# Kernel tuning notes

Hardware: AMD Instinct MI355X
Metric: run time of the kernel (lower is better)

The kernel has to match this reference:

```python
import jax, jax.numpy as jnp
import numpy as np

STATE_DIM = 1024
INPUT_DIM = 1024
BATCH = 8192


def setup_inputs() -> dict:
    key = jax.random.key(0)
    ks = jax.random.split(key, 7)
    # Kaiming-uniform-ish init like torch Linear
    bx = 1.0 / np.sqrt(INPUT_DIM)
    bh = 1.0 / np.sqrt(STATE_DIM)
    return {
        "x": jax.random.normal(ks[0], (BATCH, INPUT_DIM), jnp.float32),
        "prevh": jax.random.normal(ks[1], (BATCH, STATE_DIM), jnp.float32),
        "prevc": jax.random.normal(ks[2], (BATCH, STATE_DIM), jnp.float32),
        "Wx": jax.random.uniform(ks[3], (INPUT_DIM, 4 * STATE_DIM), jnp.float32, -bx, bx),
        "bx": jax.random.uniform(ks[4], (4 * STATE_DIM,), jnp.float32, -bx, bx),
        "Wh": jax.random.uniform(ks[5], (STATE_DIM, 4 * STATE_DIM), jnp.float32, -bh, bh),
    }


def reference(x, prevh, prevc, Wx, bx, Wh):
    # stacked gate pre-activations: [B, 4*state_dim]
    stacked = x @ Wx + bx + prevh @ Wh
    i_bar, f_bar, o_bar, g_bar = jnp.split(stacked, 4, axis=1)
    i = jax.nn.sigmoid(i_bar)
    f = jax.nn.sigmoid(f_bar)
    o = jax.nn.sigmoid(o_bar)
    g = jnp.tanh(g_bar)
    nextc = prevc * f + g * i
    nexth = jnp.tanh(nextc) * o
    return (nexth, nextc)
```

## Files before the change

kernel.cpp:

```cpp
#include <hip/hip_runtime.h>
#include <hip/hip_bf16.h>


#define BATCH   8192
#define SDIM    1024
#define KDIM    2048
#define NT      32

typedef __attribute__((ext_vector_type(8))) short s16x8;
typedef __attribute__((ext_vector_type(4))) float f32x4;

__device__ __forceinline__ void gload16(const void* g, void* l) {
    __builtin_amdgcn_global_load_lds((const __attribute__((address_space(1))) void*)g,
                                     (__attribute__((address_space(3))) void*)l,
                                     16, 0, 0);
}

__device__ __forceinline__ float fast_sigmoid(float x) {
    return 1.0f / (1.0f + __expf(-x));
}
__device__ __forceinline__ float fast_tanh(float v) {
    float a = fabsf(v);
    float e = __expf(-2.0f * a);
    float t = (1.0f - e) / (1.0f + e);
    return copysignf(t, v);
}

__global__ void convA(const float* __restrict__ x, const float* __restrict__ h,
                      __hip_bfloat16* __restrict__ A) {
    int t = blockIdx.x * blockDim.x + threadIdx.x;
    int e = t << 3;
    int b = e >> 11;
    int k = e & 2047;
    const float* src = (k < 1024) ? (x + (size_t)b * 1024 + k)
                                  : (h + (size_t)b * 1024 + (k - 1024));
    float4 v0 = *(const float4*)(src);
    float4 v1 = *(const float4*)(src + 4);
    union { __hip_bfloat16 b[8]; s16x8 v; } u;
    u.b[0] = __float2bfloat16(v0.x); u.b[1] = __float2bfloat16(v0.y);
    u.b[2] = __float2bfloat16(v0.z); u.b[3] = __float2bfloat16(v0.w);
    u.b[4] = __float2bfloat16(v1.x); u.b[5] = __float2bfloat16(v1.y);
    u.b[6] = __float2bfloat16(v1.z); u.b[7] = __float2bfloat16(v1.w);
    *(s16x8*)(A + e) = u.v;
}

__global__ void convW(const float* __restrict__ Wx, const float* __restrict__ Wh,
                      __hip_bfloat16* __restrict__ Wt) {
    __shared__ float tile[32][33];
    int k0 = blockIdx.x * 32;
    int n0 = blockIdx.y * 32;
    int tx = threadIdx.x;
    int ty = threadIdx.y;
#pragma unroll
    for (int j = 0; j < 4; ++j) {
        int k = k0 + ty + j * 8;
        int n = n0 + tx;
        float v = (k < 1024) ? Wx[(size_t)k * 4096 + n]
                             : Wh[(size_t)(k - 1024) * 4096 + n];
        tile[ty + j * 8][tx] = v;
    }
    __syncthreads();
#pragma unroll
    for (int j = 0; j < 4; ++j) {
        int n = n0 + ty + j * 8;
        int k = k0 + tx;
        int np = ((n & 1023) >> 4) * 64 + (n >> 10) * 16 + (n & 15);
        Wt[(size_t)np * 2048 + k] = __float2bfloat16(tile[tx][ty + j * 8]);
    }
}

__global__ __launch_bounds__(512, 2) void lstm_gemm(
    const __hip_bfloat16* __restrict__ A,
    const __hip_bfloat16* __restrict__ Wt,
    const float* __restrict__ bx,
    const float* __restrict__ prevc,
    float* __restrict__ outh,
    float* __restrict__ outc)
{
    __shared__ __align__(16) char lds[131072];

    const int tid  = threadIdx.x;
    const int lane = tid & 63;
    const int w    = tid >> 6;
    const int wr   = w >> 2;
    const int wc   = w & 3;
    const int l15  = lane & 15;

    const int bid = blockIdx.x;
    const int xcd = bid & 7, j = bid >> 3;
    const int mt = (xcd >> 1) * 8 + (j & 7);
    const int nt = (xcd & 1) * 8 + (j >> 3);
    const int m0 = mt * 256, n0 = nt * 256, S0 = nt * 64;

    const int scol = ((lane & 7) ^ (lane >> 3)) << 3;
    const __hip_bfloat16* Ag = A  + (size_t)m0 * KDIM;
    const __hip_bfloat16* Bg = Wt + (size_t)n0 * KDIM;

    auto SA = [&](int tt, int p) {
        char* dst = lds + (2 * (tt & 1) + p) * 16384 + w * 1024;
        const __hip_bfloat16* src =
            Ag + (size_t)(p * 128 + w * 8 + (lane >> 3)) * KDIM + tt * 64 + scol;
        gload16(src, dst);
        gload16(src + (size_t)64 * KDIM, dst + 8192);
    };
    auto SB = [&](int tt, int p) {
        char* dst = lds + 65536 + (2 * (tt & 1) + p) * 16384 + w * 1024;
        const __hip_bfloat16* src =
            Bg + (size_t)(p * 128 + w * 8 + (lane >> 3)) * KDIM + tt * 64 + scol;
        gload16(src, dst);
        gload16(src + (size_t)64 * KDIM, dst + 8192);
    };

    f32x4 acc[8][4];
#pragma unroll
    for (int m = 0; m < 8; ++m)
#pragma unroll
        for (int g = 0; g < 4; ++g)
            acc[m][g] = (f32x4)0.0f;

    SB(0, 0); SB(0, 1); SA(0, 0); SA(0, 1); SB(1, 0); SB(1, 1);
    asm volatile("s_waitcnt vmcnt(4)" ::: "memory");
    __builtin_amdgcn_s_barrier();
    __builtin_amdgcn_sched_barrier(0);

    const int swz0 = (((lane >> 4))     ^ (lane & 7)) << 4;
    const int swz1 = (((lane >> 4) | 4) ^ (lane & 7)) << 4;
    const int brow = (wc & 1) * 64;

    s16x8 afX[2][2], afY[2][2], bf[4][2];

#define LGKM(n)                                             \
    asm volatile("s_waitcnt lgkmcnt(" #n ")" ::: "memory"); \
    __builtin_amdgcn_sched_barrier(0);

#define MBLK(AF, mb)                                                          \
    __builtin_amdgcn_s_setprio(1);                                            \
    _Pragma("unroll")                                                         \
    for (int kf = 0; kf < 2; ++kf)                                            \
        _Pragma("unroll")                                                     \
        for (int mm = 0; mm < 2; ++mm)                                        \
            _Pragma("unroll")                                                 \
            for (int g = 0; g < 4; ++g)                                       \
                acc[(mb) + mm][g] = __builtin_amdgcn_mfma_f32_16x16x32_bf16(  \
                    AF[mm][kf], bf[g][kf], acc[(mb) + mm][g], 0, 0, 0);       \
    __builtin_amdgcn_s_setprio(0);

    for (int t = 0; t < NT; ++t) {
        const char* as = lds + (2 * (t & 1) + wr) * 16384;
        const char* bs = lds + 65536 + (2 * (t & 1) + (wc >> 1)) * 16384;

#pragma unroll
        for (int g = 0; g < 4; ++g) {
            bf[g][0] = *(const s16x8*)(bs + (brow + g * 16 + l15) * 128 + swz0);
            bf[g][1] = *(const s16x8*)(bs + (brow + g * 16 + l15) * 128 + swz1);
        }
#pragma unroll
        for (int mm = 0; mm < 2; ++mm) {
            afX[mm][0] = *(const s16x8*)(as + (mm * 16 + l15) * 128 + swz0);
            afX[mm][1] = *(const s16x8*)(as + (mm * 16 + l15) * 128 + swz1);
        }
#pragma unroll
        for (int mm = 0; mm < 2; ++mm) {
            afY[mm][0] = *(const s16x8*)(as + ((mm + 2) * 16 + l15) * 128 + swz0);
            afY[mm][1] = *(const s16x8*)(as + ((mm + 2) * 16 + l15) * 128 + swz1);
        }
        if (t + 1 < NT) { SA(t + 1, 0); SA(t + 1, 1); }

        LGKM(4);
        MBLK(afX, 0);

#pragma unroll
        for (int mm = 0; mm < 2; ++mm) {
            afX[mm][0] = *(const s16x8*)(as + ((mm + 4) * 16 + l15) * 128 + swz0);
            afX[mm][1] = *(const s16x8*)(as + ((mm + 4) * 16 + l15) * 128 + swz1);
        }
        LGKM(4);
        MBLK(afY, 2);

        __builtin_amdgcn_sched_barrier(0);
        __builtin_amdgcn_s_barrier();
        __builtin_amdgcn_sched_barrier(0);

        if (t + 2 < NT) { SB(t + 2, 0); SB(t + 2, 1); }
#pragma unroll
        for (int mm = 0; mm < 2; ++mm) {
            afY[mm][0] = *(const s16x8*)(as + ((mm + 6) * 16 + l15) * 128 + swz0);
            afY[mm][1] = *(const s16x8*)(as + ((mm + 6) * 16 + l15) * 128 + swz1);
        }
        LGKM(4);
        MBLK(afX, 4);

        LGKM(0);
        MBLK(afY, 6);

        __builtin_amdgcn_sched_barrier(0);
        if (t + 2 < NT) {
            asm volatile("s_waitcnt vmcnt(4)" ::: "memory");
        } else {
            asm volatile("s_waitcnt vmcnt(0)" ::: "memory");
        }
        __builtin_amdgcn_s_barrier();
        __builtin_amdgcn_sched_barrier(0);
    }
#undef LGKM
#undef MBLK

    const int st  = S0 + wc * 16 + l15;
    const float b_i = bx[st];
    const float b_f = bx[1024 + st];
    const float b_o = bx[2048 + st];
    const float b_g = bx[3072 + st];
    const int rbase = m0 + wr * 128 + (lane >> 4) * 4;

#pragma unroll
    for (int m = 0; m < 8; ++m) {
#pragma unroll
        for (int q = 0; q < 4; ++q) {
            int row = rbase + m * 16 + q;
            float ib = acc[m][0][q] + b_i;
            float fb = acc[m][1][q] + b_f;
            float ob = acc[m][2][q] + b_o;
            float gb = acc[m][3][q] + b_g;
            float ig = fast_sigmoid(ib);
            float fg = fast_sigmoid(fb);
            float og = fast_sigmoid(ob);
            float gg = fast_tanh(gb);
            float pc = prevc[(size_t)row * SDIM + st];
            float nc = pc * fg + gg * ig;
            float nh = fast_tanh(nc) * og;
            outh[(size_t)row * SDIM + st] = nh;
            outc[(size_t)row * SDIM + st] = nc;
        }
    }
}

extern "C" void kernel_launch(void* const* d_in, const int* in_sizes, int n_in,
                              void* d_out, int out_size, void* d_ws, size_t ws_size,
                              hipStream_t stream) {
    const float* x     = (const float*)d_in[0];
    const float* prevh = (const float*)d_in[1];
    const float* prevc = (const float*)d_in[2];
    const float* Wx    = (const float*)d_in[3];
    const float* bx    = (const float*)d_in[4];
    const float* Wh    = (const float*)d_in[5];

    __hip_bfloat16* Abf = (__hip_bfloat16*)d_ws;
    __hip_bfloat16* Wt  = Abf + (size_t)BATCH * KDIM;

    float* outh = (float*)d_out;
    float* outc = outh + (size_t)BATCH * SDIM;

    hipLaunchKernelGGL(convA, dim3(8192), dim3(256), 0, stream, x, prevh, Abf);
    hipLaunchKernelGGL(convW, dim3(64, 128), dim3(32, 8), 0, stream, Wx, Wh, Wt);
    hipLaunchKernelGGL(lstm_gemm, dim3(512), dim3(512), 0, stream,
                       Abf, Wt, bx, prevc, outh, outc);
}
```

Measured before the change: 156.6 us.

## Prepack weights in MFMA fragment order and load B directly to registers

The weight conversion kernel now writes Wx/Wh in the exact per-wave MFMA fragment order, so the GEMM can load B operands straight from global memory into registers, with no LDS staging. This removes B's LDS buffers and their reads, halving LDS use, and register double-buffers B across tiles. In exchange, each wave loads its own B fragments, so there is less reuse across waves in a block and more global/L2 traffic. Each iteration also waits for vmcnt(0), which may expose load latency. The weight pack kernel reads strided columns, which may be less coalesced.

Result: slower. 162.1 us (+3.5%).

```diff
diff --git a/kernel.cpp b/kernel.cpp
--- a/kernel.cpp
+++ b/kernel.cpp
@@ -44,40 +44,39 @@
     *(s16x8*)(A + e) = u.v;
 }
 
-__global__ void convW(const float* __restrict__ Wx, const float* __restrict__ Wh,
-                      __hip_bfloat16* __restrict__ Wt) {
-    __shared__ float tile[32][33];
-    int k0 = blockIdx.x * 32;
-    int n0 = blockIdx.y * 32;
-    int tx = threadIdx.x;
-    int ty = threadIdx.y;
-#pragma unroll
-    for (int j = 0; j < 4; ++j) {
-        int k = k0 + ty + j * 8;
-        int n = n0 + tx;
-        float v = (k < 1024) ? Wx[(size_t)k * 4096 + n]
-                             : Wh[(size_t)(k - 1024) * 4096 + n];
-        tile[ty + j * 8][tx] = v;
-    }
-    __syncthreads();
-#pragma unroll
-    for (int j = 0; j < 4; ++j) {
-        int n = n0 + ty + j * 8;
-        int k = k0 + tx;
-        int np = ((n & 1023) >> 4) * 64 + (n >> 10) * 16 + (n & 15);
-        Wt[(size_t)np * 2048 + k] = __float2bfloat16(tile[tx][ty + j * 8]);
-    }
+__global__ void convW2(const float* __restrict__ Wx, const float* __restrict__ Wh,
+                       __hip_bfloat16* __restrict__ Wt2) {
+    int tid  = blockIdx.x * blockDim.x + threadIdx.x;
+    int lane = tid & 63;
+    int r    = tid >> 6;
+    int kfg  = r & 7;
+    int g    = kfg >> 1;
+    int kf   = kfg & 1;
+    int r2   = r >> 3;
+    int kt   = r2 & 31;
+    int r3   = r2 >> 5;
+    int wc   = r3 & 3;
+    int ntl  = r3 >> 2;
+    int n     = g * 1024 + ntl * 64 + wc * 16 + (lane & 15);
+    int kbase = kt * 64 + kf * 32 + (lane >> 4) * 8;
+    const float* src = (kbase < 1024) ? (Wx + (size_t)kbase * 4096 + n)
+                                      : (Wh + (size_t)(kbase - 1024) * 4096 + n);
+    union { __hip_bfloat16 b[8]; s16x8 v; } u;
+#pragma unroll
+    for (int e = 0; e < 8; ++e)
+        u.b[e] = __float2bfloat16(src[(size_t)e * 4096]);
+    *(s16x8*)((char*)Wt2 + (size_t)tid * 16) = u.v;
 }
 
 __global__ __launch_bounds__(512, 2) void lstm_gemm(
     const __hip_bfloat16* __restrict__ A,
-    const __hip_bfloat16* __restrict__ Wt,
+    const __hip_bfloat16* __restrict__ Wt2,
     const float* __restrict__ bx,
     const float* __restrict__ prevc,
     float* __restrict__ outh,
     float* __restrict__ outc)
 {
-    __shared__ __align__(16) char lds[131072];
+    __shared__ __align__(16) char lds[65536];
 
     const int tid  = threadIdx.x;
     const int lane = tid & 63;
@@ -90,11 +89,10 @@
     const int xcd = bid & 7, j = bid >> 3;
     const int mt = (xcd >> 1) * 8 + (j & 7);
     const int nt = (xcd & 1) * 8 + (j >> 3);
-    const int m0 = mt * 256, n0 = nt * 256, S0 = nt * 64;
+    const int m0 = mt * 256, S0 = nt * 64;
 
     const int scol = ((lane & 7) ^ (lane >> 3)) << 3;
-    const __hip_bfloat16* Ag = A  + (size_t)m0 * KDIM;
-    const __hip_bfloat16* Bg = Wt + (size_t)n0 * KDIM;
+    const __hip_bfloat16* Ag = A + (size_t)m0 * KDIM;
 
     auto SA = [&](int tt, int p) {
         char* dst = lds + (2 * (tt & 1) + p) * 16384 + w * 1024;
@@ -103,13 +101,9 @@
         gload16(src, dst);
         gload16(src + (size_t)64 * KDIM, dst + 8192);
     };
-    auto SB = [&](int tt, int p) {
-        char* dst = lds + 65536 + (2 * (tt & 1) + p) * 16384 + w * 1024;
-        const __hip_bfloat16* src =
-            Bg + (size_t)(p * 128 + w * 8 + (lane >> 3)) * KDIM + tt * 64 + scol;
-        gload16(src, dst);
-        gload16(src + (size_t)64 * KDIM, dst + 8192);
-    };
+
+    const char* wb = (const char*)Wt2 + ((size_t)(nt * 4 + wc) * 32) * 8192
+                   + (size_t)lane * 16;
 
     f32x4 acc[8][4];
 #pragma unroll
@@ -118,22 +112,38 @@
         for (int g = 0; g < 4; ++g)
             acc[m][g] = (f32x4)0.0f;
 
-    SB(0, 0); SB(0, 1); SA(0, 0); SA(0, 1); SB(1, 0); SB(1, 1);
-    asm volatile("s_waitcnt vmcnt(4)" ::: "memory");
+    s16x8 bfA[4][2], bfB[4][2];
+    s16x8 afX[2][2], afY[2][2];
+
+#define LOADB(BF, T)                                                      \
+    _Pragma("unroll")                                                     \
+    for (int g = 0; g < 4; ++g)                                           \
+        _Pragma("unroll")                                                 \
+        for (int kf = 0; kf < 2; ++kf)                                    \
+            BF[g][kf] = *(const s16x8*)(wb + (size_t)(T) * 8192           \
+                                           + (g * 2 + kf) * 1024);
+
+    SA(0, 0); SA(0, 1);
+    LOADB(bfA, 0);
+    asm volatile("s_waitcnt vmcnt(8)" ::: "memory");
     __builtin_amdgcn_s_barrier();
     __builtin_amdgcn_sched_barrier(0);
 
     const int swz0 = (((lane >> 4))     ^ (lane & 7)) << 4;
     const int swz1 = (((lane >> 4) | 4) ^ (lane & 7)) << 4;
-    const int brow = (wc & 1) * 64;
-
-    s16x8 afX[2][2], afY[2][2], bf[4][2];
 
 #define LGKM(n)                                             \
     asm volatile("s_waitcnt lgkmcnt(" #n ")" ::: "memory"); \
     __builtin_amdgcn_sched_barrier(0);
 
-#define MBLK(AF, mb)                                                          \
+#define RD2(AF, r0)                                                           \
+    _Pragma("unroll")                                                         \
+    for (int mm = 0; mm < 2; ++mm) {                                          \
+        AF[mm][0] = *(const s16x8*)(as + (((r0) + mm) * 16 + l15) * 128 + swz0);\
+        AF[mm][1] = *(const s16x8*)(as + (((r0) + mm) * 16 + l15) * 128 + swz1);\
+    }
+
+#define MB(AF, BF, mb)                                                        \
     __builtin_amdgcn_s_setprio(1);                                            \
     _Pragma("unroll")                                                         \
     for (int kf = 0; kf < 2; ++kf)                                            \
@@ -142,68 +152,38 @@
             _Pragma("unroll")                                                 \
             for (int g = 0; g < 4; ++g)                                       \
                 acc[(mb) + mm][g] = __builtin_amdgcn_mfma_f32_16x16x32_bf16(  \
-                    AF[mm][kf], bf[g][kf], acc[(mb) + mm][g], 0, 0, 0);       \
+                    AF[mm][kf], BF[g][kf], acc[(mb) + mm][g], 0, 0, 0);       \
     __builtin_amdgcn_s_setprio(0);
 
-    for (int t = 0; t < NT; ++t) {
-        const char* as = lds + (2 * (t & 1) + wr) * 16384;
-        const char* bs = lds + 65536 + (2 * (t & 1) + (wc >> 1)) * 16384;
-
-#pragma unroll
-        for (int g = 0; g < 4; ++g) {
-            bf[g][0] = *(const s16x8*)(bs + (brow + g * 16 + l15) * 128 + swz0);
-            bf[g][1] = *(const s16x8*)(bs + (brow + g * 16 + l15) * 128 + swz1);
-        }
-#pragma unroll
-        for (int mm = 0; mm < 2; ++mm) {
-            afX[mm][0] = *(const s16x8*)(as + (mm * 16 + l15) * 128 + swz0);
-            afX[mm][1] = *(const s16x8*)(as + (mm * 16 + l15) * 128 + swz1);
-        }
-#pragma unroll
-        for (int mm = 0; mm < 2; ++mm) {
-            afY[mm][0] = *(const s16x8*)(as + ((mm + 2) * 16 + l15) * 128 + swz0);
-            afY[mm][1] = *(const s16x8*)(as + ((mm + 2) * 16 + l15) * 128 + swz1);
-        }
-        if (t + 1 < NT) { SA(t + 1, 0); SA(t + 1, 1); }
-
-        LGKM(4);
-        MBLK(afX, 0);
-
-#pragma unroll
-        for (int mm = 0; mm < 2; ++mm) {
-            afX[mm][0] = *(const s16x8*)(as + ((mm + 4) * 16 + l15) * 128 + swz0);
-            afX[mm][1] = *(const s16x8*)(as + ((mm + 4) * 16 + l15) * 128 + swz1);
-        }
-        LGKM(4);
-        MBLK(afY, 2);
-
-        __builtin_amdgcn_sched_barrier(0);
-        __builtin_amdgcn_s_barrier();
-        __builtin_amdgcn_sched_barrier(0);
-
-        if (t + 2 < NT) { SB(t + 2, 0); SB(t + 2, 1); }
-#pragma unroll
-        for (int mm = 0; mm < 2; ++mm) {
-            afY[mm][0] = *(const s16x8*)(as + ((mm + 6) * 16 + l15) * 128 + swz0);
-            afY[mm][1] = *(const s16x8*)(as + ((mm + 6) * 16 + l15) * 128 + swz1);
-        }
-        LGKM(4);
-        MBLK(afX, 4);
-
-        LGKM(0);
-        MBLK(afY, 6);
-
-        __builtin_amdgcn_sched_barrier(0);
-        if (t + 2 < NT) {
-            asm volatile("s_waitcnt vmcnt(4)" ::: "memory");
-        } else {
-            asm volatile("s_waitcnt vmcnt(0)" ::: "memory");
-        }
-        __builtin_amdgcn_s_barrier();
-        __builtin_amdgcn_sched_barrier(0);
-    }
+#define TILE(T, BFC, BFN)                                                     \
+    {                                                                         \
+        const char* as = lds + (2 * ((T) & 1) + wr) * 16384;                  \
+        if ((T) + 1 < NT) {                                                   \
+            LOADB(BFN, (T) + 1);                                              \
+            SA((T) + 1, 0); SA((T) + 1, 1);                                   \
+        }                                                                     \
+        RD2(afX, 0);                                                          \
+        RD2(afY, 2);                                                          \
+        LGKM(4); MB(afX, BFC, 0);                                             \
+        RD2(afX, 4);                                                          \
+        LGKM(4); MB(afY, BFC, 2);                                             \
+        RD2(afY, 6);                                                          \
+        LGKM(4); MB(afX, BFC, 4);                                             \
+        LGKM(0); MB(afY, BFC, 6);                                             \
+        asm volatile("s_waitcnt vmcnt(0)" ::: "memory");                      \
+        __builtin_amdgcn_s_barrier();                                         \
+        __builtin_amdgcn_sched_barrier(0);                                    \
+    }
+
+    for (int t = 0; t < NT; t += 2) {
+        TILE(t,     bfA, bfB);
+        TILE(t + 1, bfB, bfA);
+    }
+#undef TILE
+#undef MB
+#undef RD2
 #undef LGKM
-#undef MBLK
+#undef LOADB
 
     const int st  = S0 + wc * 16 + l15;
     const float b_i = bx[st];
@@ -245,13 +225,13 @@
     const float* Wh    = (const float*)d_in[5];
 
     __hip_bfloat16* Abf = (__hip_bfloat16*)d_ws;
-    __hip_bfloat16* Wt  = Abf + (size_t)BATCH * KDIM;
+    __hip_bfloat16* Wt2 = Abf + (size_t)BATCH * KDIM;
 
     float* outh = (float*)d_out;
     float* outc = outh + (size_t)BATCH * SDIM;
 
     hipLaunchKernelGGL(convA, dim3(8192), dim3(256), 0, stream, x, prevh, Abf);
-    hipLaunchKernelGGL(convW, dim3(64, 128), dim3(32, 8), 0, stream, Wx, Wh, Wt);
+    hipLaunchKernelGGL(convW2, dim3(4096), dim3(256), 0, stream, Wx, Wh, Wt2);
     hipLaunchKernelGGL(lstm_gemm, dim3(512), dim3(512), 0, stream,
-                       Abf, Wt, bx, prevc, outh, outc);
-}
+                       Abf, Wt2, bx, prevc, outh, outc);
+}
```
